# Performance work log

Measured on AMD Instinct MI355X. Metric: run time of the kernel, lower is better.

## Reference

```python
import jax, jax.numpy as jnp
import numpy as np

B, L, C = 32, 128, 21
PATCH, STRIDE = 16, 16
E, H, HEADS = 128, 128, 8
NLAYERS = 2
KSIZE = 3
PRED = 96
N = (L - PATCH) // STRIDE + 1  # 8 patches


def setup_inputs() -> dict:
    key = jax.random.key(0)
    ks = jax.random.split(key, 24)
    g = lambda i, shape, s=0.05: jax.random.normal(ks[i], shape, jnp.float32) * s
    return {
        'x': g(0, (B, L, C), 1.0),
        'embed_W': g(1, (E, PATCH)), 'embed_b': g(2, (E,)),
        'ln_g': jnp.ones((E,), jnp.float32), 'ln_b': jnp.zeros((E,), jnp.float32),
        'qW': g(3, (E, E)), 'qb': g(4, (E,)),
        'kW': g(5, (E, E)), 'kb': g(6, (E,)),
        'vW': g(7, (E, E)), 'vb': g(8, (E,)),
        'lstm_Wx': g(9, (NLAYERS, 4 * H, E)), 'lstm_Wh': g(10, (NLAYERS, 4 * H, H)), 'lstm_b': g(11, (NLAYERS, 4 * H)),
        'conv_W': g(12, (E, E, KSIZE)), 'conv_b': g(13, (E,)),
        'ssm_W': g(14, (E, E)), 'ssm_b': g(15, (E,)),
        'outp_W': g(16, (E, E)), 'outp_b': g(17, (E,)),
        'proj_W': g(18, (PRED, E)), 'proj_b': g(19, (PRED,)),
    }


def _layernorm(x, g, b, eps=1e-5):
    m = x.mean(-1, keepdims=True)
    v = ((x - m) ** 2).mean(-1, keepdims=True)
    return (x - m) * jax.lax.rsqrt(v + eps) * g + b


def _xlstm_dqn(ctx, Wx, Wh, bias):
    # DQNxLSTM: re-runs a 2-layer LSTM over the FULL sequence L times,
    # carrying (h,c) across iterations; returns the outputs of the last pass.
    ctx_T = jnp.swapaxes(ctx, 0, 1)  # [N, Bc, E]
    Bc = ctx.shape[0]
    h0 = jnp.zeros((NLAYERS, Bc, H), ctx.dtype)
    c0 = jnp.zeros_like(h0)

    def cell(carry, x_t):  # x_t: [Bc, E]
        h, c = carry
        inp = x_t
        hs, cs = [], []
        for l in range(NLAYERS):
            gates = inp @ Wx[l].T + h[l] @ Wh[l].T + bias[l]  # [Bc, 4H]
            i, f, g_, o = jnp.split(gates, 4, axis=-1)
            c_new = jax.nn.sigmoid(f) * c[l] + jax.nn.sigmoid(i) * jnp.tanh(g_)
            h_new = jax.nn.sigmoid(o) * jnp.tanh(c_new)
            hs.append(h_new); cs.append(c_new)
            inp = h_new
        return (jnp.stack(hs), jnp.stack(cs)), inp

    def outer(carry, _):
        carry2, outs = jax.lax.scan(cell, carry, ctx_T)  # outs: [N, Bc, H]
        return carry2, outs

    _, all_outs = jax.lax.scan(outer, (h0, c0), None, length=N)
    return jnp.swapaxes(all_outs[-1], 0, 1)  # [Bc, N, H]


def _conv1d_same(x, W, b):  # x: [Bc, N, E]
    y = jax.lax.conv_general_dilated(
        jnp.swapaxes(x, 1, 2), W, (1,), 'SAME',
        dimension_numbers=('NCH', 'OIH', 'NCH'))
    return jnp.swapaxes(y + b[None, :, None], 1, 2)


def reference(x, embed_W, embed_b, ln_g, ln_b, qW, qb, kW, kb, vW, vb,
              lstm_Wx, lstm_Wh, lstm_b, conv_W, conv_b, ssm_W, ssm_b,
              outp_W, outp_b, proj_W, proj_b):
    Bc = B * C
    # channel independence: b l c -> (b c) l
    xc = jnp.swapaxes(x, 1, 2).reshape(Bc, L)
    # patching (unfold)
    idx = jnp.arange(N)[:, None] * STRIDE + jnp.arange(PATCH)[None, :]
    patches = xc[:, idx]  # [Bc, N, PATCH]
    emb = patches @ embed_W.T + embed_b  # [Bc, N, E]
    xn = _layernorm(emb, ln_g, ln_b)
    # attention (faithful to original, incl. scale by sqrt(E) and bhnl,bhnd->bhnd einsum)
    d = E // HEADS
    q = (xn @ qW.T + qb).reshape(Bc, N, HEADS, d).transpose(0, 2, 1, 3)
    k = (xn @ kW.T + kb).reshape(Bc, N, HEADS, d).transpose(0, 2, 1, 3)
    v = (xn @ vW.T + vb).reshape(Bc, N, HEADS, d).transpose(0, 2, 1, 3)
    attn = jax.nn.softmax(jnp.einsum('bhnd,bhld->bhnl', q, k) / (E ** 0.5), axis=-1)
    ctx = jnp.einsum('bhnl,bhnd->bhnd', attn, v)  # as in original (elementwise-in-n)
    ctx = ctx.transpose(0, 2, 1, 3).reshape(Bc, N, E)
    ctx = _xlstm_dqn(ctx, lstm_Wx, lstm_Wh, lstm_b)
    ctx = _conv1d_same(ctx, conv_W, conv_b)
    ctx = ctx @ ssm_W.T + ssm_b
    ctx = ctx @ outp_W.T + outp_b
    ctx = ctx + xn  # residual onto the normed input (as in original)
    y = ctx @ proj_W.T + proj_b  # [Bc, N, PRED]
    return y
```

## Files before the change

### kernel.cpp

```cpp
#include <hip/hip_runtime.h>

typedef unsigned short ushort_t;
typedef unsigned int uint_t;

using bf16x8 = __attribute__((ext_vector_type(8))) short;
using f32x4  = __attribute__((ext_vector_type(4))) float;

__device__ __forceinline__ ushort_t f2b(float f){
    union { float f; uint_t u; } v; v.f = f;
    uint_t u = v.u;
    uint_t r = (u + 0x7FFFu + ((u >> 16) & 1u)) >> 16;
    return (ushort_t)r;
}

__global__ void prep_k(const float* __restrict__ vW, const float* __restrict__ Wx,
                       const float* __restrict__ Wh, const float* __restrict__ cW,
                       const float* __restrict__ sW, const float* __restrict__ oW,
                       const float* __restrict__ pW, const float* __restrict__ x,
                       ushort_t* __restrict__ wb, float* __restrict__ xT)
{
    int idx = blockIdx.x * 256 + threadIdx.x;
    switch (blockIdx.y){
    case 0: if (idx < 16384) wb[idx]          = f2b(vW[idx]);           break;
    case 1: if (idx < 65536) wb[16384  + idx] = f2b(Wx[idx]);           break;
    case 2: if (idx < 65536) wb[81920  + idx] = f2b(Wh[idx]);           break;
    case 3: if (idx < 65536) wb[147456 + idx] = f2b(Wx[65536 + idx]);   break;
    case 4: if (idx < 65536) wb[212992 + idx] = f2b(Wh[65536 + idx]);   break;
    case 5: if (idx < 49152){
                int k = idx >> 14; int oi = idx & 16383;
                wb[278528 + idx] = f2b(cW[oi * 3 + k]);
            } break;
    case 6: if (idx < 16384) wb[327680 + idx] = f2b(sW[idx]);           break;
    case 7: if (idx < 16384) wb[344064 + idx] = f2b(oW[idx]);           break;
    case 8: if (idx < 12288) wb[360448 + idx] = f2b(pW[idx]);           break;
    case 9:
        for (int i = idx; i < 86016; i += 65536){
            int bc = i >> 7, l = i & 127;
            int b = bc / 21, c = bc % 21;
            xT[i] = x[(b * 128 + l) * 21 + c];
        }
        break;
    }
}

__global__ __launch_bounds__(64) void head_k(
    const float* __restrict__ xT, const float* __restrict__ eW,
    const float* __restrict__ eb, const float* __restrict__ lng,
    const float* __restrict__ lnb, const ushort_t* __restrict__ vWb,
    const float* __restrict__ vb, const ushort_t* __restrict__ wx0b,
    const float* __restrict__ lb, float* __restrict__ xnF, float* __restrict__ X0F)
{
    __shared__ ushort_t xnL[2048];
    __shared__ ushort_t c0L[2048];

    const int lane = threadIdx.x;
    const int rowbase = blockIdx.x * 16;
    const int e0 = lane, e1 = lane + 64;

    float w0[16], w1[16];
#pragma unroll
    for (int p = 0; p < 16; ++p){ w0[p] = eW[e0 * 16 + p]; w1[p] = eW[e1 * 16 + p]; }
    const float bi0 = eb[e0], bi1 = eb[e1];
    const float ga0 = lng[e0], ga1 = lng[e1];
    const float be0 = lnb[e0], be1 = lnb[e1];

    for (int i = 0; i < 16; ++i){
        const int row = rowbase + i;
        const int bc = row >> 3, n = row & 7;
        const float* xp = xT + bc * 128 + n * 16;
        float v0 = bi0, v1 = bi1;
#pragma unroll
        for (int p = 0; p < 16; ++p){
            float pv = xp[p];
            v0 += w0[p] * pv; v1 += w1[p] * pv;
        }
        float s = v0 + v1, sq = v0 * v0 + v1 * v1;
#pragma unroll
        for (int m = 32; m >= 1; m >>= 1){
            s  += __shfl_xor(s,  m);
            sq += __shfl_xor(sq, m);
        }
        float mean = s * (1.f / 128.f);
        float var  = sq * (1.f / 128.f) - mean * mean;
        float r    = rsqrtf(var + 1e-5f);
        float y0 = (v0 - mean) * r * ga0 + be0;
        float y1 = (v1 - mean) * r * ga1 + be1;
        xnF[row * 128 + e0] = y0;
        xnF[row * 128 + e1] = y1;
        const int sz = (i & 7) << 3;
        xnL[i * 128 + (e0 ^ sz)] = f2b(y0);
        xnL[i * 128 + (e1 ^ sz)] = f2b(y1);
    }

    const int r0 = lane & 15, g = lane >> 4, sw = r0 & 7;
    {
        bf16x8 a[4];
#pragma unroll
        for (int kt = 0; kt < 4; ++kt)
            a[kt] = *(const bf16x8*)(&xnL[r0 * 128 + ((kt * 32 + g * 8) ^ (sw << 3))]);
#pragma unroll
        for (int nt = 0; nt < 8; ++nt){
            const int col = nt * 16 + r0;
            float bv = vb[col];
            f32x4 acc = {bv, bv, bv, bv};
#pragma unroll
            for (int kt = 0; kt < 4; ++kt)
                acc = __builtin_amdgcn_mfma_f32_16x16x32_bf16(
                        a[kt], *(const bf16x8*)(vWb + col * 128 + kt * 32 + g * 8), acc, 0, 0, 0);
#pragma unroll
            for (int q = 0; q < 4; ++q){
                int rr = g * 4 + q;
                c0L[rr * 128 + (col ^ ((rr & 7) << 3))] = f2b(acc[q]);
            }
        }
    }
    {
        bf16x8 a[4];
#pragma unroll
        for (int kt = 0; kt < 4; ++kt)
            a[kt] = *(const bf16x8*)(&c0L[r0 * 128 + ((kt * 32 + g * 8) ^ (sw << 3))]);
        for (int nt = 0; nt < 32; ++nt){
            const int col = nt * 16 + r0;
            float bv = lb[col];
            f32x4 acc = {bv, bv, bv, bv};
#pragma unroll
            for (int kt = 0; kt < 4; ++kt)
                acc = __builtin_amdgcn_mfma_f32_16x16x32_bf16(
                        a[kt], *(const bf16x8*)(wx0b + col * 128 + kt * 32 + g * 8), acc, 0, 0, 0);
#pragma unroll
            for (int q = 0; q < 4; ++q)
                X0F[(rowbase + g * 4 + q) * 512 + col] = acc[q];
        }
    }
}

__global__ __launch_bounds__(512, 2) void lstm_f2(
    const float* __restrict__ X0, const ushort_t* __restrict__ Wh0,
    const ushort_t* __restrict__ Wx1, const ushort_t* __restrict__ Wh1,
    const float* __restrict__ lb, ushort_t* __restrict__ outB)
{
    extern __shared__ ushort_t smem[];
    ushort_t* hbuf = smem;
    ushort_t* wxs  = smem + 8192;

    const int tid = threadIdx.x;
    const int wid = tid >> 6, lane = tid & 63;
    const int r0 = lane & 15, g = lane >> 4;
    const int sw = r0 & 7;
    const int bcb = blockIdx.x * 16;
    const float K1 = 1.44269504f, K2 = 2.88539008f;

    for (int i = tid; i < 8192; i += 512) hbuf[i] = 0;
    for (int idx = tid; idx < 8192; idx += 512){
        int col = idx >> 4, c = idx & 15;
        *(bf16x8*)(wxs + col * 128 + ((c ^ (col & 7)) << 3)) =
            *(const bf16x8*)(Wx1 + col * 128 + c * 8);
    }

    bf16x8 wh0[4][4], wh1[4][4];
#pragma unroll
    for (int t4 = 0; t4 < 4; ++t4){
        const int cb = t4 * 128 + wid * 16;
#pragma unroll
        for (int kt = 0; kt < 4; ++kt){
            wh0[t4][kt] = *(const bf16x8*)(Wh0 + (cb + r0) * 128 + kt * 32 + g * 8);
            wh1[t4][kt] = *(const bf16x8*)(Wh1 + (cb + r0) * 128 + kt * 32 + g * 8);
        }
    }
    float b1v[4];
#pragma unroll
    for (int t4 = 0; t4 < 4; ++t4) b1v[t4] = lb[512 + t4 * 128 + wid * 16 + r0];

    const char* adr[4];
#pragma unroll
    for (int kt = 0; kt < 4; ++kt)
        adr[kt] = (const char*)hbuf + r0 * 256 + (((kt * 32 + g * 8) ^ (sw << 3)) << 1);
    char* wrq[4];
#pragma unroll
    for (int q = 0; q < 4; ++q){
        int row = g * 4 + q;
        wrq[q] = (char*)hbuf + row * 256 + (((wid * 16 + r0) ^ ((row & 7) << 3)) << 1);
    }
    const char* wxp[4][2];
    {
        const int e = (sw >> 2) * 64;
#pragma unroll
        for (int t4 = 0; t4 < 4; ++t4){
            const char* base = (const char*)wxs
                + (t4 * 128 + wid * 16 + r0) * 256 + ((g ^ (sw & 3)) * 16);
            wxp[t4][0] = base + e;
            wxp[t4][1] = base + (64 - e);
        }
    }
    const char* xp[4];
#pragma unroll
    for (int q = 0; q < 4; ++q)
        xp[q] = (const char*)(X0 + (bcb + g * 4 + q) * 4096 + wid * 16 + r0) + 2048;
    int tnn = 1;

    float c0[4] = {0,0,0,0}, c1[4] = {0,0,0,0};

    f32x4 acc[4];
#pragma unroll
    for (int t4 = 0; t4 < 4; ++t4)
#pragma unroll
        for (int q = 0; q < 4; ++q)
            acc[t4][q] = *(const float*)(xp[q] - 2048 + t4 * 512);

    __syncthreads();

#pragma unroll 1
    for (int tt = 0; tt < 32; ++tt){
#pragma unroll
        for (int pp = 0; pp < 2; ++pp){
            const int ph = tt * 2 + pp;
            const int RDO = (pp ^ 1) * 4096;
            const int WRO = pp * 4096;

            bf16x8 a0[4], ah[4];
#pragma unroll
            for (int kt = 0; kt < 4; ++kt){
                a0[kt] = *(const bf16x8*)(adr[kt] + RDO);
                ah[kt] = *(const bf16x8*)(adr[kt] + 8192 + RDO);
            }

#pragma unroll
            for (int kt = 0; kt < 4; ++kt)
#pragma unroll
                for (int t4 = 0; t4 < 4; ++t4)
                    acc[t4] = __builtin_amdgcn_mfma_f32_16x16x32_bf16(a0[kt], wh0[t4][kt], acc[t4], 0, 0, 0);

#pragma unroll
            for (int q = 0; q < 4; ++q){
                float iv = acc[0][q], fv = acc[1][q], gv = acc[2][q], ov = acc[3][q];
                float af = 1.f + __builtin_amdgcn_exp2f(-K1 * fv);
                float ai = 1.f + __builtin_amdgcn_exp2f(-K1 * iv);
                float bg = 1.f + __builtin_amdgcn_exp2f( K2 * gv);
                float cn = c0[q] * __builtin_amdgcn_rcpf(af)
                         + (bg - 2.f) * __builtin_amdgcn_rcpf(ai * bg);
                c0[q] = cn;
                float ao = 1.f + __builtin_amdgcn_exp2f(-K1 * ov);
                float bc = 1.f + __builtin_amdgcn_exp2f( K2 * cn);
                float hv = (bc - 2.f) * __builtin_amdgcn_rcpf(ao * bc);
                *(ushort_t*)(wrq[q] + WRO) = f2b(hv);
            }

            if (ph > 0){
                f32x4 accB[4];
#pragma unroll
                for (int t4 = 0; t4 < 4; ++t4){
                    f32x4 tmp = {b1v[t4], b1v[t4], b1v[t4], b1v[t4]};
                    accB[t4] = tmp;
                }
#pragma unroll
                for (int kt = 0; kt < 4; ++kt)
#pragma unroll
                    for (int t4 = 0; t4 < 4; ++t4){
                        bf16x8 wx = *(const bf16x8*)(wxp[t4][kt & 1] + ((kt >> 1) << 7));
                        accB[t4] = __builtin_amdgcn_mfma_f32_16x16x32_bf16(a0[kt], wx,          accB[t4], 0, 0, 0);
                        accB[t4] = __builtin_amdgcn_mfma_f32_16x16x32_bf16(ah[kt], wh1[t4][kt], accB[t4], 0, 0, 0);
                    }
#pragma unroll
                for (int q = 0; q < 4; ++q){
                    float iv = accB[0][q], fv = accB[1][q], gv = accB[2][q], ov = accB[3][q];
                    float af = 1.f + __builtin_amdgcn_exp2f(-K1 * fv);
                    float ai = 1.f + __builtin_amdgcn_exp2f(-K1 * iv);
                    float bg = 1.f + __builtin_amdgcn_exp2f( K2 * gv);
                    float cn = c1[q] * __builtin_amdgcn_rcpf(af)
                             + (bg - 2.f) * __builtin_amdgcn_rcpf(ai * bg);
                    c1[q] = cn;
                    float ao = 1.f + __builtin_amdgcn_exp2f(-K1 * ov);
                    float bc = 1.f + __builtin_amdgcn_exp2f( K2 * cn);
                    float hv = (bc - 2.f) * __builtin_amdgcn_rcpf(ao * bc);
                    *(ushort_t*)(wrq[q] + 8192 + WRO) = f2b(hv);
                    if (ph >= 57){
                        int row = g * 4 + q;
                        outB[((bcb + row) * 8 + ((ph - 1) & 7)) * 128 + wid * 16 + r0] = f2b(hv);
                    }
                }
            }

            if (ph < 63){
#pragma unroll
                for (int t4 = 0; t4 < 4; ++t4)
#pragma unroll
                    for (int q = 0; q < 4; ++q)
                        acc[t4][q] = *(const float*)(xp[q] + t4 * 512);
                long d = (tnn == 7) ? -14336L : 2048L;
                tnn = (tnn == 7) ? 0 : tnn + 1;
#pragma unroll
                for (int q = 0; q < 4; ++q) xp[q] += d;
            }
            __syncthreads();
        }
    }

    {
        bf16x8 a0[4], ah[4];
#pragma unroll
        for (int kt = 0; kt < 4; ++kt){
            a0[kt] = *(const bf16x8*)(adr[kt] + 4096);
            ah[kt] = *(const bf16x8*)(adr[kt] + 8192 + 4096);
        }
        f32x4 acc2[4];
#pragma unroll
        for (int t4 = 0; t4 < 4; ++t4){
            f32x4 tmp = {b1v[t4], b1v[t4], b1v[t4], b1v[t4]};
            acc2[t4] = tmp;
        }
#pragma unroll
        for (int kt = 0; kt < 4; ++kt)
#pragma unroll
            for (int t4 = 0; t4 < 4; ++t4){
                bf16x8 wx = *(const bf16x8*)(wxp[t4][kt & 1] + ((kt >> 1) << 7));
                acc2[t4] = __builtin_amdgcn_mfma_f32_16x16x32_bf16(a0[kt], wx,          acc2[t4], 0, 0, 0);
                acc2[t4] = __builtin_amdgcn_mfma_f32_16x16x32_bf16(ah[kt], wh1[t4][kt], acc2[t4], 0, 0, 0);
            }
#pragma unroll
        for (int q = 0; q < 4; ++q){
            float iv = acc2[0][q], fv = acc2[1][q], gv = acc2[2][q], ov = acc2[3][q];
            float af = 1.f + __builtin_amdgcn_exp2f(-K1 * fv);
            float ai = 1.f + __builtin_amdgcn_exp2f(-K1 * iv);
            float bg = 1.f + __builtin_amdgcn_exp2f( K2 * gv);
            float cn = c1[q] * __builtin_amdgcn_rcpf(af)
                     + (bg - 2.f) * __builtin_amdgcn_rcpf(ai * bg);
            float ao = 1.f + __builtin_amdgcn_exp2f(-K1 * ov);
            float bc = 1.f + __builtin_amdgcn_exp2f( K2 * cn);
            float hv = (bc - 2.f) * __builtin_amdgcn_rcpf(ao * bc);
            int row = g * 4 + q;
            outB[((bcb + row) * 8 + 7) * 128 + wid * 16 + r0] = f2b(hv);
        }
    }
}

__global__ __launch_bounds__(256) void tail_k(
    const ushort_t* __restrict__ ls, const ushort_t* __restrict__ cWk,
    const float* __restrict__ cbias, const ushort_t* __restrict__ sW,
    const float* __restrict__ sbias, const ushort_t* __restrict__ oW,
    const float* __restrict__ obias, const float* __restrict__ xnF,
    const ushort_t* __restrict__ pW, const float* __restrict__ pbias,
    float* __restrict__ out)
{
    __shared__ ushort_t bufA[8192];
    __shared__ ushort_t bufB[8192];
    const int lane = threadIdx.x & 63, wave = threadIdx.x >> 6;
    const int r0 = lane & 15, g = lane >> 4;
    const int rowbase = blockIdx.x * 64;
    const int lr0 = wave * 16;

    {
        const int n = r0 & 7;
        bf16x8 a[3][4];
#pragma unroll
        for (int k = 0; k < 3; ++k){
            bool valid = (n + k >= 1) && (n + k <= 8);
            const ushort_t* ap = ls + (rowbase + lr0 + r0 + k - 1) * 128 + g * 8;
#pragma unroll
            for (int kt = 0; kt < 4; ++kt){
                bf16x8 z = {0,0,0,0,0,0,0,0};
                a[k][kt] = valid ? *(const bf16x8*)(ap + kt * 32) : z;
            }
        }
#pragma unroll
        for (int nt = 0; nt < 8; ++nt){
            const int col = nt * 16 + r0;
            float bv = cbias[col];
            f32x4 acc = {bv, bv, bv, bv};
#pragma unroll
            for (int k = 0; k < 3; ++k)
#pragma unroll
                for (int kt = 0; kt < 4; ++kt)
                    acc = __builtin_amdgcn_mfma_f32_16x16x32_bf16(
                            a[k][kt], *(const bf16x8*)(cWk + k * 16384 + col * 128 + kt * 32 + g * 8),
                            acc, 0, 0, 0);
#pragma unroll
            for (int q = 0; q < 4; ++q){
                int row = lr0 + g * 4 + q;
                bufA[row * 128 + (col ^ ((row & 7) << 3))] = f2b(acc[q]);
            }
        }
    }
    __syncthreads();
    {
        bf16x8 a[4];
#pragma unroll
        for (int kt = 0; kt < 4; ++kt)
            a[kt] = *(const bf16x8*)(&bufA[(lr0 + r0) * 128 + ((kt * 32 + g * 8) ^ ((r0 & 7) << 3))]);
#pragma unroll
        for (int nt = 0; nt < 8; ++nt){
            const int col = nt * 16 + r0;
            float bv = sbias[col];
            f32x4 acc = {bv, bv, bv, bv};
#pragma unroll
            for (int kt = 0; kt < 4; ++kt)
                acc = __builtin_amdgcn_mfma_f32_16x16x32_bf16(
                        a[kt], *(const bf16x8*)(sW + col * 128 + kt * 32 + g * 8), acc, 0, 0, 0);
#pragma unroll
            for (int q = 0; q < 4; ++q){
                int row = lr0 + g * 4 + q;
                bufB[row * 128 + (col ^ ((row & 7) << 3))] = f2b(acc[q]);
            }
        }
    }
    __syncthreads();
    {
        bf16x8 a[4];
#pragma unroll
        for (int kt = 0; kt < 4; ++kt)
            a[kt] = *(const bf16x8*)(&bufB[(lr0 + r0) * 128 + ((kt * 32 + g * 8) ^ ((r0 & 7) << 3))]);
#pragma unroll
        for (int nt = 0; nt < 8; ++nt){
            const int col = nt * 16 + r0;
            float bv = obias[col];
            f32x4 acc = {bv, bv, bv, bv};
#pragma unroll
            for (int kt = 0; kt < 4; ++kt)
                acc = __builtin_amdgcn_mfma_f32_16x16x32_bf16(
                        a[kt], *(const bf16x8*)(oW + col * 128 + kt * 32 + g * 8), acc, 0, 0, 0);
#pragma unroll
            for (int q = 0; q < 4; ++q){
                int row = lr0 + g * 4 + q;
                float v = acc[q] + xnF[(rowbase + row) * 128 + col];
                bufA[row * 128 + (col ^ ((row & 7) << 3))] = f2b(v);
            }
        }
    }
    __syncthreads();
    {
        bf16x8 a[4];
#pragma unroll
        for (int kt = 0; kt < 4; ++kt)
            a[kt] = *(const bf16x8*)(&bufA[(lr0 + r0) * 128 + ((kt * 32 + g * 8) ^ ((r0 & 7) << 3))]);
#pragma unroll
        for (int nt = 0; nt < 6; ++nt){
            const int col = nt * 16 + r0;
            float bv = pbias[col];
            f32x4 acc = {bv, bv, bv, bv};
#pragma unroll
            for (int kt = 0; kt < 4; ++kt)
                acc = __builtin_amdgcn_mfma_f32_16x16x32_bf16(
                        a[kt], *(const bf16x8*)(pW + col * 128 + kt * 32 + g * 8), acc, 0, 0, 0);
#pragma unroll
            for (int q = 0; q < 4; ++q)
                out[(rowbase + lr0 + g * 4 + q) * 96 + col] = acc[q];
        }
    }
}

extern "C" void kernel_launch(void* const* d_in, const int* in_sizes, int n_in,
                              void* d_out, int out_size, void* d_ws, size_t ws_size,
                              hipStream_t stream)
{
    const float* x   = (const float*)d_in[0];
    const float* eW  = (const float*)d_in[1];
    const float* eb  = (const float*)d_in[2];
    const float* lng = (const float*)d_in[3];
    const float* lnb = (const float*)d_in[4];
    const float* vW  = (const float*)d_in[9];
    const float* vb  = (const float*)d_in[10];
    const float* Wx  = (const float*)d_in[11];
    const float* Wh  = (const float*)d_in[12];
    const float* lb  = (const float*)d_in[13];
    const float* cW  = (const float*)d_in[14];
    const float* cb_ = (const float*)d_in[15];
    const float* sW  = (const float*)d_in[16];
    const float* sb  = (const float*)d_in[17];
    const float* oW  = (const float*)d_in[18];
    const float* ob  = (const float*)d_in[19];
    const float* pW  = (const float*)d_in[20];
    const float* pb  = (const float*)d_in[21];

    char* ws = (char*)d_ws;
    float*    xnF = (float*)   (ws + 0);
    float*    X0F = (float*)   (ws + 5505024);
    ushort_t* lsB = (ushort_t*)(ws + 16515072);
    ushort_t* wb  = (ushort_t*)(ws + 17891328);
    float*    xT  = (float*)   (ws + 18874368);

    hipFuncSetAttribute((const void*)lstm_f2,
                        hipFuncAttributeMaxDynamicSharedMemorySize, 147456);

    prep_k<<<dim3(256, 10), 256, 0, stream>>>(vW, Wx, Wh, cW, sW, oW, pW, x, wb, xT);
    head_k<<<336, 64, 0, stream>>>(xT, eW, eb, lng, lnb, wb + 0, vb, wb + 16384, lb,
                                   xnF, X0F);
    lstm_f2<<<42, 512, 147456, stream>>>(X0F, wb + 81920, wb + 147456, wb + 212992,
                                         lb, lsB);
    tail_k<<<84, 256, 0, stream>>>(lsB, wb + 278528, cb_, wb + 327680, sb,
                                   wb + 344064, ob, xnF, wb + 360448, pb, (float*)d_out);
}
```

Baseline: 206.8 us.

## Halve LSTM block to 4 waves holding all recurrent weights in registers

The LSTM recurrence kernel now runs 256 threads per block instead of 512. Each wave handles 32 hidden columns (8 MFMA tiles) and keeps Wh0, Wh1 and Wx1 all in VGPRs, so the layer-1 input weights are no longer staged in dynamic shared memory. Layer-0 and layer-1 MFMAs are interleaved per k-slice, which lets the layer-1 matmul overlap layer-0 work and cuts block-wide barrier participants. The cost is very high register pressure (96 bf16x8 weight fragments plus accumulators), which risks spills, and fewer waves are available to hide latency.

```diff
diff --git a/kernel.cpp b/kernel.cpp
--- a/kernel.cpp
+++ b/kernel.cpp
@@ -134,78 +134,64 @@
     }
 }
 
-__global__ __launch_bounds__(512, 2) void lstm_f2(
+__global__ __launch_bounds__(256, 1) void lstm_f4(
     const float* __restrict__ X0, const ushort_t* __restrict__ Wh0,
     const ushort_t* __restrict__ Wx1, const ushort_t* __restrict__ Wh1,
     const float* __restrict__ lb, ushort_t* __restrict__ outB)
 {
-    extern __shared__ ushort_t smem[];
-    ushort_t* hbuf = smem;
-    ushort_t* wxs  = smem + 8192;
+    __shared__ ushort_t hbuf[8192];
 
     const int tid = threadIdx.x;
-    const int wid = tid >> 6, lane = tid & 63;
+    const int w = tid >> 6, lane = tid & 63;
     const int r0 = lane & 15, g = lane >> 4;
     const int sw = r0 & 7;
     const int bcb = blockIdx.x * 16;
     const float K1 = 1.44269504f, K2 = 2.88539008f;
 
-    for (int i = tid; i < 8192; i += 512) hbuf[i] = 0;
-    for (int idx = tid; idx < 8192; idx += 512){
-        int col = idx >> 4, c = idx & 15;
-        *(bf16x8*)(wxs + col * 128 + ((c ^ (col & 7)) << 3)) =
-            *(const bf16x8*)(Wx1 + col * 128 + c * 8);
-    }
-
-    bf16x8 wh0[4][4], wh1[4][4];
-#pragma unroll
-    for (int t4 = 0; t4 < 4; ++t4){
-        const int cb = t4 * 128 + wid * 16;
+    for (int i = tid; i < 8192; i += 256) hbuf[i] = 0;
+
+    bf16x8 wh0[8][4], wh1[8][4], wx1[8][4];
+#pragma unroll
+    for (int t8 = 0; t8 < 8; ++t8){
+        const int col = (t8 >> 1) * 128 + w * 32 + (t8 & 1) * 16 + r0;
 #pragma unroll
         for (int kt = 0; kt < 4; ++kt){
-            wh0[t4][kt] = *(const bf16x8*)(Wh0 + (cb + r0) * 128 + kt * 32 + g * 8);
-            wh1[t4][kt] = *(const bf16x8*)(Wh1 + (cb + r0) * 128 + kt * 32 + g * 8);
-        }
-    }
-    float b1v[4];
-#pragma unroll
-    for (int t4 = 0; t4 < 4; ++t4) b1v[t4] = lb[512 + t4 * 128 + wid * 16 + r0];
-
-    const char* adr[4];
-#pragma unroll
-    for (int kt = 0; kt < 4; ++kt)
-        adr[kt] = (const char*)hbuf + r0 * 256 + (((kt * 32 + g * 8) ^ (sw << 3)) << 1);
-    char* wrq[4];
-#pragma unroll
-    for (int q = 0; q < 4; ++q){
-        int row = g * 4 + q;
-        wrq[q] = (char*)hbuf + row * 256 + (((wid * 16 + r0) ^ ((row & 7) << 3)) << 1);
-    }
-    const char* wxp[4][2];
-    {
-        const int e = (sw >> 2) * 64;
-#pragma unroll
-        for (int t4 = 0; t4 < 4; ++t4){
-            const char* base = (const char*)wxs
-                + (t4 * 128 + wid * 16 + r0) * 256 + ((g ^ (sw & 3)) * 16);
-            wxp[t4][0] = base + e;
-            wxp[t4][1] = base + (64 - e);
-        }
+            wh0[t8][kt] = *(const bf16x8*)(Wh0 + col * 128 + kt * 32 + g * 8);
+            wh1[t8][kt] = *(const bf16x8*)(Wh1 + col * 128 + kt * 32 + g * 8);
+            wx1[t8][kt] = *(const bf16x8*)(Wx1 + col * 128 + kt * 32 + g * 8);
+        }
+    }
+    float b1v[8];
+#pragma unroll
+    for (int t8 = 0; t8 < 8; ++t8)
+        b1v[t8] = lb[512 + (t8 >> 1) * 128 + w * 32 + (t8 & 1) * 16 + r0];
+
+    char* wrq[8];
+#pragma unroll
+    for (int wq = 0; wq < 8; ++wq){
+        const int q = wq & 3, ct = wq >> 2;
+        const int row = g * 4 + q;
+        const int col = w * 32 + ct * 16 + r0;
+        wrq[wq] = (char*)hbuf + row * 256 + ((col ^ ((row & 7) << 3)) << 1);
     }
     const char* xp[4];
 #pragma unroll
     for (int q = 0; q < 4; ++q)
-        xp[q] = (const char*)(X0 + (bcb + g * 4 + q) * 4096 + wid * 16 + r0) + 2048;
+        xp[q] = (const char*)(X0 + (bcb + g * 4 + q) * 4096 + w * 32 + r0);
+
+    float c0[8], c1[8];
+#pragma unroll
+    for (int i = 0; i < 8; ++i){ c0[i] = 0.f; c1[i] = 0.f; }
+
+    f32x4 acc[8], accB[8];
+#pragma unroll
+    for (int t8 = 0; t8 < 8; ++t8)
+#pragma unroll
+        for (int q = 0; q < 4; ++q)
+            acc[t8][q] = *(const float*)(xp[q] + (((t8 >> 1) * 128 + (t8 & 1) * 16) << 2));
+#pragma unroll
+    for (int q = 0; q < 4; ++q) xp[q] += 2048;
     int tnn = 1;
-
-    float c0[4] = {0,0,0,0}, c1[4] = {0,0,0,0};
-
-    f32x4 acc[4];
-#pragma unroll
-    for (int t4 = 0; t4 < 4; ++t4)
-#pragma unroll
-        for (int q = 0; q < 4; ++q)
-            acc[t4][q] = *(const float*)(xp[q] - 2048 + t4 * 512);
 
     __syncthreads();
 
@@ -217,118 +203,125 @@
             const int RDO = (pp ^ 1) * 4096;
             const int WRO = pp * 4096;
 
-            bf16x8 a0[4], ah[4];
+            if (ph > 0){
+#pragma unroll
+                for (int t8 = 0; t8 < 8; ++t8){
+                    f32x4 tmp = {b1v[t8], b1v[t8], b1v[t8], b1v[t8]};
+                    accB[t8] = tmp;
+                }
+            }
+
 #pragma unroll
             for (int kt = 0; kt < 4; ++kt){
-                a0[kt] = *(const bf16x8*)(adr[kt] + RDO);
-                ah[kt] = *(const bf16x8*)(adr[kt] + 8192 + RDO);
-            }
-
-#pragma unroll
-            for (int kt = 0; kt < 4; ++kt)
-#pragma unroll
-                for (int t4 = 0; t4 < 4; ++t4)
-                    acc[t4] = __builtin_amdgcn_mfma_f32_16x16x32_bf16(a0[kt], wh0[t4][kt], acc[t4], 0, 0, 0);
-
-#pragma unroll
-            for (int q = 0; q < 4; ++q){
-                float iv = acc[0][q], fv = acc[1][q], gv = acc[2][q], ov = acc[3][q];
-                float af = 1.f + __builtin_amdgcn_exp2f(-K1 * fv);
-                float ai = 1.f + __builtin_amdgcn_exp2f(-K1 * iv);
-                float bg = 1.f + __builtin_amdgcn_exp2f( K2 * gv);
-                float cn = c0[q] * __builtin_amdgcn_rcpf(af)
-                         + (bg - 2.f) * __builtin_amdgcn_rcpf(ai * bg);
-                c0[q] = cn;
-                float ao = 1.f + __builtin_amdgcn_exp2f(-K1 * ov);
-                float bc = 1.f + __builtin_amdgcn_exp2f( K2 * cn);
-                float hv = (bc - 2.f) * __builtin_amdgcn_rcpf(ao * bc);
-                *(ushort_t*)(wrq[q] + WRO) = f2b(hv);
-            }
-
-            if (ph > 0){
-                f32x4 accB[4];
-#pragma unroll
-                for (int t4 = 0; t4 < 4; ++t4){
-                    f32x4 tmp = {b1v[t4], b1v[t4], b1v[t4], b1v[t4]};
-                    accB[t4] = tmp;
+                const char* ab = (const char*)hbuf + r0 * 256
+                               + (((kt * 32 + g * 8) ^ (sw << 3)) << 1);
+                bf16x8 a0 = *(const bf16x8*)(ab + RDO);
+                bf16x8 ah = *(const bf16x8*)(ab + 8192 + RDO);
+#pragma unroll
+                for (int t8 = 0; t8 < 8; ++t8)
+                    acc[t8] = __builtin_amdgcn_mfma_f32_16x16x32_bf16(a0, wh0[t8][kt], acc[t8], 0, 0, 0);
+                if (ph > 0){
+#pragma unroll
+                    for (int t8 = 0; t8 < 8; ++t8){
+                        accB[t8] = __builtin_amdgcn_mfma_f32_16x16x32_bf16(a0, wx1[t8][kt], accB[t8], 0, 0, 0);
+                        accB[t8] = __builtin_amdgcn_mfma_f32_16x16x32_bf16(ah, wh1[t8][kt], accB[t8], 0, 0, 0);
+                    }
                 }
-#pragma unroll
-                for (int kt = 0; kt < 4; ++kt)
-#pragma unroll
-                    for (int t4 = 0; t4 < 4; ++t4){
-                        bf16x8 wx = *(const bf16x8*)(wxp[t4][kt & 1] + ((kt >> 1) << 7));
-                        accB[t4] = __builtin_amdgcn_mfma_f32_16x16x32_bf16(a0[kt], wx,          accB[t4], 0, 0, 0);
-                        accB[t4] = __builtin_amdgcn_mfma_f32_16x16x32_bf16(ah[kt], wh1[t4][kt], accB[t4], 0, 0, 0);
-                    }
+            }
+
+            if (ph < 64){
+#pragma unroll
+                for (int ct = 0; ct < 2; ++ct)
 #pragma unroll
                 for (int q = 0; q < 4; ++q){
-                    float iv = accB[0][q], fv = accB[1][q], gv = accB[2][q], ov = accB[3][q];
+                    float iv = acc[ct][q], fv = acc[2 + ct][q];
+                    float gv = acc[4 + ct][q], ov = acc[6 + ct][q];
                     float af = 1.f + __builtin_amdgcn_exp2f(-K1 * fv);
                     float ai = 1.f + __builtin_amdgcn_exp2f(-K1 * iv);
                     float bg = 1.f + __builtin_amdgcn_exp2f( K2 * gv);
-                    float cn = c1[q] * __builtin_amdgcn_rcpf(af)
+                    float cn = c0[ct * 4 + q] * __builtin_amdgcn_rcpf(af)
                              + (bg - 2.f) * __builtin_amdgcn_rcpf(ai * bg);
-                    c1[q] = cn;
+                    c0[ct * 4 + q] = cn;
                     float ao = 1.f + __builtin_amdgcn_exp2f(-K1 * ov);
                     float bc = 1.f + __builtin_amdgcn_exp2f( K2 * cn);
                     float hv = (bc - 2.f) * __builtin_amdgcn_rcpf(ao * bc);
-                    *(ushort_t*)(wrq[q] + 8192 + WRO) = f2b(hv);
+                    *(ushort_t*)(wrq[ct * 4 + q] + WRO) = f2b(hv);
+                }
+                if (ph < 63){
+#pragma unroll
+                    for (int t8 = 0; t8 < 8; ++t8)
+#pragma unroll
+                        for (int q = 0; q < 4; ++q)
+                            acc[t8][q] = *(const float*)(xp[q] + (((t8 >> 1) * 128 + (t8 & 1) * 16) << 2));
+                    long d = (tnn == 7) ? -14336L : 2048L;
+                    tnn = (tnn == 7) ? 0 : tnn + 1;
+#pragma unroll
+                    for (int q = 0; q < 4; ++q) xp[q] += d;
+                }
+            }
+
+            if (ph > 0){
+#pragma unroll
+                for (int ct = 0; ct < 2; ++ct)
+#pragma unroll
+                for (int q = 0; q < 4; ++q){
+                    float iv = accB[ct][q], fv = accB[2 + ct][q];
+                    float gv = accB[4 + ct][q], ov = accB[6 + ct][q];
+                    float af = 1.f + __builtin_amdgcn_exp2f(-K1 * fv);
+                    float ai = 1.f + __builtin_amdgcn_exp2f(-K1 * iv);
+                    float bg = 1.f + __builtin_amdgcn_exp2f( K2 * gv);
+                    float cn = c1[ct * 4 + q] * __builtin_amdgcn_rcpf(af)
+                             + (bg - 2.f) * __builtin_amdgcn_rcpf(ai * bg);
+                    c1[ct * 4 + q] = cn;
+                    float ao = 1.f + __builtin_amdgcn_exp2f(-K1 * ov);
+                    float bc = 1.f + __builtin_amdgcn_exp2f( K2 * cn);
+                    float hv = (bc - 2.f) * __builtin_amdgcn_rcpf(ao * bc);
+                    *(ushort_t*)(wrq[ct * 4 + q] + 8192 + WRO) = f2b(hv);
                     if (ph >= 57){
                         int row = g * 4 + q;
-                        outB[((bcb + row) * 8 + ((ph - 1) & 7)) * 128 + wid * 16 + r0] = f2b(hv);
+                        outB[((bcb + row) * 8 + ((ph - 1) & 7)) * 128 + w * 32 + ct * 16 + r0] = f2b(hv);
                     }
                 }
             }
-
-            if (ph < 63){
-#pragma unroll
-                for (int t4 = 0; t4 < 4; ++t4)
-#pragma unroll
-                    for (int q = 0; q < 4; ++q)
-                        acc[t4][q] = *(const float*)(xp[q] + t4 * 512);
-                long d = (tnn == 7) ? -14336L : 2048L;
-                tnn = (tnn == 7) ? 0 : tnn + 1;
-#pragma unroll
-                for (int q = 0; q < 4; ++q) xp[q] += d;
-            }
             __syncthreads();
         }
     }
 
     {
-        bf16x8 a0[4], ah[4];
+        f32x4 acc2[8];
+#pragma unroll
+        for (int t8 = 0; t8 < 8; ++t8){
+            f32x4 tmp = {b1v[t8], b1v[t8], b1v[t8], b1v[t8]};
+            acc2[t8] = tmp;
+        }
 #pragma unroll
         for (int kt = 0; kt < 4; ++kt){
-            a0[kt] = *(const bf16x8*)(adr[kt] + 4096);
-            ah[kt] = *(const bf16x8*)(adr[kt] + 8192 + 4096);
-        }
-        f32x4 acc2[4];
-#pragma unroll
-        for (int t4 = 0; t4 < 4; ++t4){
-            f32x4 tmp = {b1v[t4], b1v[t4], b1v[t4], b1v[t4]};
-            acc2[t4] = tmp;
-        }
-#pragma unroll
-        for (int kt = 0; kt < 4; ++kt)
-#pragma unroll
-            for (int t4 = 0; t4 < 4; ++t4){
-                bf16x8 wx = *(const bf16x8*)(wxp[t4][kt & 1] + ((kt >> 1) << 7));
-                acc2[t4] = __builtin_amdgcn_mfma_f32_16x16x32_bf16(a0[kt], wx,          acc2[t4], 0, 0, 0);
-                acc2[t4] = __builtin_amdgcn_mfma_f32_16x16x32_bf16(ah[kt], wh1[t4][kt], acc2[t4], 0, 0, 0);
-            }
+            const char* ab = (const char*)hbuf + r0 * 256
+                           + (((kt * 32 + g * 8) ^ (sw << 3)) << 1);
+            bf16x8 a0 = *(const bf16x8*)(ab + 4096);
+            bf16x8 ah = *(const bf16x8*)(ab + 8192 + 4096);
+#pragma unroll
+            for (int t8 = 0; t8 < 8; ++t8){
+                acc2[t8] = __builtin_amdgcn_mfma_f32_16x16x32_bf16(a0, wx1[t8][kt], acc2[t8], 0, 0, 0);
+                acc2[t8] = __builtin_amdgcn_mfma_f32_16x16x32_bf16(ah, wh1[t8][kt], acc2[t8], 0, 0, 0);
+            }
+        }
+#pragma unroll
+        for (int ct = 0; ct < 2; ++ct)
 #pragma unroll
         for (int q = 0; q < 4; ++q){
-            float iv = acc2[0][q], fv = acc2[1][q], gv = acc2[2][q], ov = acc2[3][q];
+            float iv = acc2[ct][q], fv = acc2[2 + ct][q];
+            float gv = acc2[4 + ct][q], ov = acc2[6 + ct][q];
             float af = 1.f + __builtin_amdgcn_exp2f(-K1 * fv);
             float ai = 1.f + __builtin_amdgcn_exp2f(-K1 * iv);
             float bg = 1.f + __builtin_amdgcn_exp2f( K2 * gv);
-            float cn = c1[q] * __builtin_amdgcn_rcpf(af)
+            float cn = c1[ct * 4 + q] * __builtin_amdgcn_rcpf(af)
                      + (bg - 2.f) * __builtin_amdgcn_rcpf(ai * bg);
             float ao = 1.f + __builtin_amdgcn_exp2f(-K1 * ov);
             float bc = 1.f + __builtin_amdgcn_exp2f( K2 * cn);
             float hv = (bc - 2.f) * __builtin_amdgcn_rcpf(ao * bc);
             int row = g * 4 + q;
-            outB[((bcb + row) * 8 + 7) * 128 + wid * 16 + r0] = f2b(hv);
+            outB[((bcb + row) * 8 + 7) * 128 + w * 32 + ct * 16 + r0] = f2b(hv);
         }
     }
 }
@@ -477,14 +470,11 @@
     ushort_t* wb  = (ushort_t*)(ws + 17891328);
     float*    xT  = (float*)   (ws + 18874368);
 
-    hipFuncSetAttribute((const void*)lstm_f2,
-                        hipFuncAttributeMaxDynamicSharedMemorySize, 147456);
-
     prep_k<<<dim3(256, 10), 256, 0, stream>>>(vW, Wx, Wh, cW, sW, oW, pW, x, wb, xT);
     head_k<<<336, 64, 0, stream>>>(xT, eW, eb, lng, lnb, wb + 0, vb, wb + 16384, lb,
                                    xnF, X0F);
-    lstm_f2<<<42, 512, 147456, stream>>>(X0F, wb + 81920, wb + 147456, wb + 212992,
-                                         lb, lsB);
+    lstm_f4<<<42, 256, 0, stream>>>(X0F, wb + 81920, wb + 147456, wb + 212992,
+                                    lb, lsB);
     tail_k<<<84, 256, 0, stream>>>(lsB, wb + 278528, cb_, wb + 327680, sb,
                                    wb + 344064, ob, xnF, wb + 360448, pb, (float*)d_out);
 }
```

New measurement: 486.4 us. 135% more time.
